# Performance work log

Hardware: AMD Instinct MI355X
Metric: run time of the kernel (lower is better)

## Reference

```python
import jax, jax.numpy as jnp
import numpy as np

ENC_DIM, PRED_DIM, JOINT_DIM, VOCAB = 512, 640, 512, 1024

def setup_inputs() -> dict:
    key = jax.random.key(0)
    ks = jax.random.split(key, 8)
    s = lambda d: 1.0 / np.sqrt(d)
    return {
        "enc_out": jax.random.normal(ks[0], (8, 256, ENC_DIM), jnp.float32),
        "pred_out": jax.random.normal(ks[1], (8, 64, PRED_DIM), jnp.float32),
        "W_enc": jax.random.uniform(ks[2], (ENC_DIM, JOINT_DIM), jnp.float32, -s(ENC_DIM), s(ENC_DIM)),
        "b_enc": jax.random.uniform(ks[3], (JOINT_DIM,), jnp.float32, -s(ENC_DIM), s(ENC_DIM)),
        "W_pred": jax.random.uniform(ks[4], (PRED_DIM, JOINT_DIM), jnp.float32, -s(PRED_DIM), s(PRED_DIM)),
        "b_pred": jax.random.uniform(ks[5], (JOINT_DIM,), jnp.float32, -s(PRED_DIM), s(PRED_DIM)),
        "W_joint": jax.random.uniform(ks[6], (JOINT_DIM, VOCAB), jnp.float32, -s(JOINT_DIM), s(JOINT_DIM)),
        "b_joint": jax.random.uniform(ks[7], (VOCAB,), jnp.float32, -s(JOINT_DIM), s(JOINT_DIM)),
    }

def reference(enc_out, pred_out, W_enc, b_enc, W_pred, b_pred, W_joint, b_joint):
    # (B,T,J) and (B,U,J) projections
    enc_p = jnp.einsum('btd,dj->btj', enc_out, W_enc) + b_enc
    pred_p = jnp.einsum('bud,dj->buj', pred_out, W_pred) + b_pred
    # broadcast add -> (B,T,U,J), tanh, project to vocab
    joint = jnp.tanh(enc_p[:, :, None, :] + pred_p[:, None, :, :])
    logits = jnp.einsum('btuj,jv->btuv', joint, W_joint) + b_joint
    return logits
```

## Files before the change

### kernel.cpp

```cpp
#include <hip/hip_runtime.h>
#include <hip/hip_bf16.h>
#include <stdint.h>

#define B_    8
#define T_    256
#define U_    64
#define JD    512
#define VD    1024
#define ROWS  (B_*T_*U_)
#define MTOT  (B_*T_)
#define UROWS (B_*U_)

typedef __attribute__((ext_vector_type(8))) short short8;
typedef __attribute__((ext_vector_type(4))) float f32x4;

__device__ __forceinline__ unsigned short f2bf(float f) {
  unsigned u = __float_as_uint(f);
  u += 0x7fffu + ((u >> 16) & 1u);
  return (unsigned short)(u >> 16);
}
__device__ __forceinline__ float fast_tanh(float x) {
  float e = __builtin_amdgcn_exp2f(x * 2.8853900817779268f);
  return 1.0f - 2.0f * __builtin_amdgcn_rcpf(e + 1.0f);
}

__global__ void __launch_bounds__(256) k_pack_w(
    const float* __restrict__ W, unsigned short* __restrict__ dst,
    int K, int N) {
  int t = blockIdx.x * blockDim.x + threadIdx.x;
  int total = (K * N) >> 3;
  if (t >= total) return;
  int lane = t & 63;
  int rest = t >> 6;
  int kch  = K >> 5;
  int kc   = rest % kch;
  int nt   = rest / kch;
  int krow = (kc << 5) + ((lane >> 4) << 3);
  int col  = (nt << 4) + (lane & 15);
  unsigned short v[8];
#pragma unroll
  for (int j = 0; j < 8; ++j) v[j] = f2bf(W[(size_t)(krow + j) * N + col]);
  uint4 o;
  o.x = v[0] | ((unsigned)v[1] << 16);
  o.y = v[2] | ((unsigned)v[3] << 16);
  o.z = v[4] | ((unsigned)v[5] << 16);
  o.w = v[6] | ((unsigned)v[7] << 16);
  *(uint4*)(dst + ((size_t)t << 3)) = o;
}

__global__ void __launch_bounds__(256) k_proj(
    const float* __restrict__ A, const unsigned short* __restrict__ Bp,
    const float* __restrict__ bias, float* __restrict__ C,
    int M, int K, int N) {
  int w    = (blockIdx.x * blockDim.x + threadIdx.x) >> 6;
  int lane = threadIdx.x & 63;
  int nw   = N >> 6;
  int wm   = w / nw, wn = w % nw;
  int m0   = wm << 4, n0 = wn << 6;
  if (m0 >= M) return;
  int kch = K >> 5;
  int q = lane >> 4, c = lane & 15;
  f32x4 acc[4] = {f32x4{0,0,0,0}, f32x4{0,0,0,0}, f32x4{0,0,0,0}, f32x4{0,0,0,0}};
  const float* arow = A + (size_t)(m0 + c) * K + (q << 3);
  for (int kc = 0; kc < kch; ++kc) {
    float4 a0 = *(const float4*)(arow + (kc << 5));
    float4 a1 = *(const float4*)(arow + (kc << 5) + 4);
    short8 a;
    a[0] = (short)f2bf(a0.x); a[1] = (short)f2bf(a0.y);
    a[2] = (short)f2bf(a0.z); a[3] = (short)f2bf(a0.w);
    a[4] = (short)f2bf(a1.x); a[5] = (short)f2bf(a1.y);
    a[6] = (short)f2bf(a1.z); a[7] = (short)f2bf(a1.w);
#pragma unroll
    for (int j = 0; j < 4; ++j) {
      size_t nt16 = (size_t)((n0 >> 4) + j);
      short8 b = *(const short8*)(Bp + (((nt16 * kch + kc) << 6) + lane) * 8);
      acc[j] = __builtin_amdgcn_mfma_f32_16x16x32_bf16(a, b, acc[j], 0, 0, 0);
    }
  }
#pragma unroll
  for (int j = 0; j < 4; ++j) {
    int col = n0 + (j << 4) + c;
    float bv = bias[col];
#pragma unroll
    for (int r = 0; r < 4; ++r) {
      int row = m0 + (q << 2) + r;
      C[(size_t)row * N + col] = acc[j][r] + bv;
    }
  }
}

__global__ void __launch_bounds__(256) k_tanh_pack(
    const float* __restrict__ enc_p, const float* __restrict__ pred_p,
    unsigned short* __restrict__ Ap) {
  int t    = blockIdx.x * blockDim.x + threadIdx.x;
  int lane = t & 63;
  int F    = t >> 6;
  int rb   = F >> 4, kc = F & 15;
  int r    = (rb << 4) + (lane & 15);
  int k0   = (kc << 5) + ((lane >> 4) << 3);
  const float* ep = enc_p  + ((size_t)(r >> 6) << 9) + k0;
  const float* pp = pred_p + ((size_t)(((r >> 14) << 6) + (r & 63)) << 9) + k0;
  float4 e0 = *(const float4*)ep, e1 = *(const float4*)(ep + 4);
  float4 p0 = *(const float4*)pp, p1 = *(const float4*)(pp + 4);
  unsigned short v[8];
  v[0] = f2bf(fast_tanh(e0.x + p0.x));
  v[1] = f2bf(fast_tanh(e0.y + p0.y));
  v[2] = f2bf(fast_tanh(e0.z + p0.z));
  v[3] = f2bf(fast_tanh(e0.w + p0.w));
  v[4] = f2bf(fast_tanh(e1.x + p1.x));
  v[5] = f2bf(fast_tanh(e1.y + p1.y));
  v[6] = f2bf(fast_tanh(e1.z + p1.z));
  v[7] = f2bf(fast_tanh(e1.w + p1.w));
  uint4 o;
  o.x = v[0] | ((unsigned)v[1] << 16);
  o.y = v[2] | ((unsigned)v[3] << 16);
  o.z = v[4] | ((unsigned)v[5] << 16);
  o.w = v[6] | ((unsigned)v[7] << 16);
  *(uint4*)(Ap + ((size_t)t << 3)) = o;
}

__global__ void __launch_bounds__(256) k_gemm3(
    const unsigned short* __restrict__ Ap, const unsigned short* __restrict__ Bp,
    const float* __restrict__ bias, float* __restrict__ out) {
  int bid  = blockIdx.x;
  int nt   = bid & 7;
  int mt   = bid >> 3;
  int w    = threadIdx.x >> 6, lane = threadIdx.x & 63;
  int wm   = w >> 1, wn = w & 1;
  int rb0  = (mt << 3) + (wm << 2);
  int nt0  = (nt << 3) + (wn << 2);
  const short8* a8 = (const short8*)Ap;
  const short8* b8 = (const short8*)Bp;

  f32x4 acc[4][4];
#pragma unroll
  for (int i = 0; i < 4; ++i)
#pragma unroll
    for (int j = 0; j < 4; ++j) acc[i][j] = f32x4{0, 0, 0, 0};

  short8 a[4], b[4], an[4], bn[4];
#pragma unroll
  for (int i = 0; i < 4; ++i) {
    a[i] = a8[(((size_t)(rb0 + i) * 16 + 0) << 6) + lane];
    b[i] = b8[(((size_t)(nt0 + i) * 16 + 0) << 6) + lane];
  }
#pragma unroll
  for (int kc = 0; kc < 16; ++kc) {
    if (kc < 15) {
#pragma unroll
      for (int i = 0; i < 4; ++i) {
        an[i] = a8[(((size_t)(rb0 + i) * 16 + kc + 1) << 6) + lane];
        bn[i] = b8[(((size_t)(nt0 + i) * 16 + kc + 1) << 6) + lane];
      }
    }
#pragma unroll
    for (int i = 0; i < 4; ++i)
#pragma unroll
      for (int j = 0; j < 4; ++j)
        acc[i][j] = __builtin_amdgcn_mfma_f32_16x16x32_bf16(a[i], b[j], acc[i][j], 0, 0, 0);
#pragma unroll
    for (int i = 0; i < 4; ++i) { a[i] = an[i]; b[i] = bn[i]; }
  }

  int q = lane >> 4, c = lane & 15;
#pragma unroll
  for (int j = 0; j < 4; ++j) {
    int col = ((nt0 + j) << 4) + c;
    float bv = bias[col];
#pragma unroll
    for (int i = 0; i < 4; ++i) {
      int row = ((rb0 + i) << 4) + (q << 2);
      size_t o = ((size_t)row << 10) + col;
#pragma unroll
      for (int r = 0; r < 4; ++r)
        out[o + ((size_t)r << 10)] = acc[i][j][r] + bv;
    }
  }
}

__global__ void __launch_bounds__(256) k_proj_naive(
    const float* __restrict__ A, const float* __restrict__ W,
    const float* __restrict__ bias, float* __restrict__ C,
    int M, int K, int N) {
  int t = blockIdx.x * blockDim.x + threadIdx.x;
  if (t >= M * N) return;
  int row = t / N, col = t % N;
  float s = bias[col];
  for (int k = 0; k < K; ++k)
    s += A[(size_t)row * K + k] * W[(size_t)k * N + col];
  C[t] = s;
}
__global__ void __launch_bounds__(256) k_joint_naive(
    const float* __restrict__ enc_p, const float* __restrict__ pred_p,
    const float* __restrict__ Wj, const float* __restrict__ bj,
    float* __restrict__ out) {
  __shared__ float jrow[JD];
  int gr = blockIdx.x;
  int bt = gr >> 6;
  int bu = ((gr >> 14) << 6) + (gr & 63);
  for (int k = threadIdx.x; k < JD; k += 256)
    jrow[k] = fast_tanh(enc_p[(size_t)bt * JD + k] + pred_p[(size_t)bu * JD + k]);
  __syncthreads();
  int v0 = threadIdx.x * 4;
  float s0 = bj[v0], s1 = bj[v0 + 1], s2 = bj[v0 + 2], s3 = bj[v0 + 3];
  for (int k = 0; k < JD; ++k) {
    float jv = jrow[k];
    const float* wr = Wj + (size_t)k * VD + v0;
    s0 += jv * wr[0];
    s1 += jv * wr[1];
    s2 += jv * wr[2];
    s3 += jv * wr[3];
  }
  size_t o = ((size_t)gr << 10) + v0;
  out[o] = s0; out[o + 1] = s1; out[o + 2] = s2; out[o + 3] = s3;
}

extern "C" void kernel_launch(void* const* d_in, const int* in_sizes, int n_in,
                              void* d_out, int out_size, void* d_ws, size_t ws_size,
                              hipStream_t stream) {
  const float* enc_out  = (const float*)d_in[0];
  const float* pred_out = (const float*)d_in[1];
  const float* W_enc    = (const float*)d_in[2];
  const float* b_enc    = (const float*)d_in[3];
  const float* W_pred   = (const float*)d_in[4];
  const float* b_pred   = (const float*)d_in[5];
  const float* W_joint  = (const float*)d_in[6];
  const float* b_joint  = (const float*)d_in[7];
  float* out = (float*)d_out;

  char* ws = (char*)d_ws;
  size_t off = 0;
  auto alloc = [&](size_t bytes) -> char* {
    char* p = ws + off;
    off += (bytes + 255) & ~(size_t)255;
    return p;
  };
  float* enc_p  = (float*)alloc((size_t)MTOT * JD * 4);
  float* pred_p = (float*)alloc((size_t)UROWS * JD * 4);
  size_t small_need = off;
  unsigned short* Wenc_p  = (unsigned short*)alloc((size_t)512 * 512 * 2);
  unsigned short* Wpred_p = (unsigned short*)alloc((size_t)640 * 512 * 2);
  unsigned short* Wjnt_p  = (unsigned short*)alloc((size_t)512 * 1024 * 2);
  unsigned short* Ap      = (unsigned short*)alloc((size_t)ROWS * JD * 2);
  size_t big_need = off;

  if (ws_size >= big_need) {
    k_pack_w<<<(512 * 512 / 8) / 256, 256, 0, stream>>>(W_enc, Wenc_p, 512, 512);
    k_pack_w<<<(640 * 512 / 8) / 256, 256, 0, stream>>>(W_pred, Wpred_p, 640, 512);
    k_pack_w<<<(512 * 1024 / 8) / 256, 256, 0, stream>>>(W_joint, Wjnt_p, 512, 1024);
    k_proj<<<(MTOT / 16) * (JD / 64) / 4, 256, 0, stream>>>(enc_out, Wenc_p, b_enc, enc_p, MTOT, 512, JD);
    k_proj<<<(UROWS / 16) * (JD / 64) / 4, 256, 0, stream>>>(pred_out, Wpred_p, b_pred, pred_p, UROWS, 640, JD);
    k_tanh_pack<<<((size_t)ROWS * JD / 8) / 256, 256, 0, stream>>>(enc_p, pred_p, Ap);
    k_gemm3<<<(ROWS / 128) * (VD / 128), 256, 0, stream>>>(Ap, Wjnt_p, b_joint, out);
  } else if (ws_size >= small_need) {
    k_proj_naive<<<(MTOT * JD + 255) / 256, 256, 0, stream>>>(enc_out, W_enc, b_enc, enc_p, MTOT, 512, JD);
    k_proj_naive<<<(UROWS * JD + 255) / 256, 256, 0, stream>>>(pred_out, W_pred, b_pred, pred_p, UROWS, 640, JD);
    k_joint_naive<<<ROWS, 256, 0, stream>>>(enc_p, pred_p, W_joint, b_joint, out);
  }
  (void)in_sizes; (void)n_in; (void)out_size;
}
```

Baseline: 959.4 us.

## Fuse tanh-pack into joint GEMM via LDS staging and merge small launches

The broadcast-add plus tanh plus bf16 pack is now computed per block into shared memory, chunk by chunk, inside the joint GEMM. This removes the large materialized Ap buffer and its global write and re-read. The three weight-pack launches and the two projection launches are each merged into a single kernel to cut launch overhead. The fused kernel uses 512-thread blocks with 128x256 tiles and syncthreads between the staging and MFMA phases. Tanh work is recomputed for each of the 4 N-tiles, and there is no double buffering, so staging may serialize with compute.

```diff
diff --git a/kernel.cpp b/kernel.cpp
--- a/kernel.cpp
+++ b/kernel.cpp
@@ -24,12 +24,9 @@
   return 1.0f - 2.0f * __builtin_amdgcn_rcpf(e + 1.0f);
 }
 
-__global__ void __launch_bounds__(256) k_pack_w(
-    const float* __restrict__ W, unsigned short* __restrict__ dst,
-    int K, int N) {
-  int t = blockIdx.x * blockDim.x + threadIdx.x;
-  int total = (K * N) >> 3;
-  if (t >= total) return;
+__device__ __forceinline__ void pack_w_body(const float* __restrict__ W,
+                                            unsigned short* __restrict__ dst,
+                                            int K, int N, int t) {
   int lane = t & 63;
   int rest = t >> 6;
   int kch  = K >> 5;
@@ -48,15 +45,24 @@
   *(uint4*)(dst + ((size_t)t << 3)) = o;
 }
 
-__global__ void __launch_bounds__(256) k_proj(
-    const float* __restrict__ A, const unsigned short* __restrict__ Bp,
-    const float* __restrict__ bias, float* __restrict__ C,
-    int M, int K, int N) {
-  int w    = (blockIdx.x * blockDim.x + threadIdx.x) >> 6;
-  int lane = threadIdx.x & 63;
-  int nw   = N >> 6;
-  int wm   = w / nw, wn = w % nw;
-  int m0   = wm << 4, n0 = wn << 6;
+__global__ void __launch_bounds__(256) k_pack_all(
+    const float* __restrict__ We, const float* __restrict__ Wp,
+    const float* __restrict__ Wj,
+    unsigned short* __restrict__ de, unsigned short* __restrict__ dp,
+    unsigned short* __restrict__ dj) {
+  int blk = blockIdx.x;
+  int tid = threadIdx.x;
+  if (blk < 128)      pack_w_body(We, de, 512, 512,  blk * 256 + tid);
+  else if (blk < 288) pack_w_body(Wp, dp, 640, 512,  (blk - 128) * 256 + tid);
+  else                pack_w_body(Wj, dj, 512, 1024, (blk - 288) * 256 + tid);
+}
+
+__device__ __forceinline__ void proj_body(const float* __restrict__ A,
+    const unsigned short* __restrict__ Bp, const float* __restrict__ bias,
+    float* __restrict__ C, int M, int K, int N, int w, int lane) {
+  int nw = N >> 6;
+  int wm = w / nw, wn = w % nw;
+  int m0 = wm << 4, n0 = wn << 6;
   if (m0 >= M) return;
   int kch = K >> 5;
   int q = lane >> 4, c = lane & 15;
@@ -89,48 +95,38 @@
   }
 }
 
-__global__ void __launch_bounds__(256) k_tanh_pack(
+__global__ void __launch_bounds__(256) k_proj_both(
+    const float* __restrict__ enc_out, const float* __restrict__ pred_out,
+    const unsigned short* __restrict__ Wep, const unsigned short* __restrict__ Wpp,
+    const float* __restrict__ b_enc, const float* __restrict__ b_pred,
+    float* __restrict__ enc_p, float* __restrict__ pred_p) {
+  int blk  = blockIdx.x;
+  int lane = threadIdx.x & 63;
+  int wloc = threadIdx.x >> 6;
+  if (blk < 256)
+    proj_body(enc_out,  Wep, b_enc,  enc_p,  MTOT,  512, JD, blk * 4 + wloc, lane);
+  else
+    proj_body(pred_out, Wpp, b_pred, pred_p, UROWS, 640, JD, (blk - 256) * 4 + wloc, lane);
+}
+
+__global__ void __launch_bounds__(512, 4) k_fused(
     const float* __restrict__ enc_p, const float* __restrict__ pred_p,
-    unsigned short* __restrict__ Ap) {
-  int t    = blockIdx.x * blockDim.x + threadIdx.x;
-  int lane = t & 63;
-  int F    = t >> 6;
-  int rb   = F >> 4, kc = F & 15;
-  int r    = (rb << 4) + (lane & 15);
-  int k0   = (kc << 5) + ((lane >> 4) << 3);
-  const float* ep = enc_p  + ((size_t)(r >> 6) << 9) + k0;
-  const float* pp = pred_p + ((size_t)(((r >> 14) << 6) + (r & 63)) << 9) + k0;
-  float4 e0 = *(const float4*)ep, e1 = *(const float4*)(ep + 4);
-  float4 p0 = *(const float4*)pp, p1 = *(const float4*)(pp + 4);
-  unsigned short v[8];
-  v[0] = f2bf(fast_tanh(e0.x + p0.x));
-  v[1] = f2bf(fast_tanh(e0.y + p0.y));
-  v[2] = f2bf(fast_tanh(e0.z + p0.z));
-  v[3] = f2bf(fast_tanh(e0.w + p0.w));
-  v[4] = f2bf(fast_tanh(e1.x + p1.x));
-  v[5] = f2bf(fast_tanh(e1.y + p1.y));
-  v[6] = f2bf(fast_tanh(e1.z + p1.z));
-  v[7] = f2bf(fast_tanh(e1.w + p1.w));
-  uint4 o;
-  o.x = v[0] | ((unsigned)v[1] << 16);
-  o.y = v[2] | ((unsigned)v[3] << 16);
-  o.z = v[4] | ((unsigned)v[5] << 16);
-  o.w = v[6] | ((unsigned)v[7] << 16);
-  *(uint4*)(Ap + ((size_t)t << 3)) = o;
-}
-
-__global__ void __launch_bounds__(256) k_gemm3(
-    const unsigned short* __restrict__ Ap, const unsigned short* __restrict__ Bp,
-    const float* __restrict__ bias, float* __restrict__ out) {
+    const unsigned short* __restrict__ Bp, const float* __restrict__ bias,
+    float* __restrict__ out) {
+  __shared__ unsigned short Alds[32 * 64 * 8];
+  const short8* a8 = (const short8*)Alds;
+  const short8* b8 = (const short8*)Bp;
+
   int bid  = blockIdx.x;
-  int nt   = bid & 7;
-  int mt   = bid >> 3;
-  int w    = threadIdx.x >> 6, lane = threadIdx.x & 63;
-  int wm   = w >> 1, wn = w & 1;
-  int rb0  = (mt << 3) + (wm << 2);
-  int nt0  = (nt << 3) + (wn << 2);
-  const short8* a8 = (const short8*)Ap;
-  const short8* b8 = (const short8*)Bp;
+  int nt   = bid & 3;
+  int mt   = bid >> 2;
+  int tid  = threadIdx.x;
+  int lane = tid & 63;
+  int w    = tid >> 6;
+  int wm   = w >> 2, wn = w & 3;
+  int rb0w = wm << 2;
+  int nt0w = (nt << 4) + (wn << 2);
+  int c15  = lane & 15, q8 = (lane >> 4) << 3;
 
   f32x4 acc[4][4];
 #pragma unroll
@@ -138,42 +134,66 @@
 #pragma unroll
     for (int j = 0; j < 4; ++j) acc[i][j] = f32x4{0, 0, 0, 0};
 
-  short8 a[4], b[4], an[4], bn[4];
-#pragma unroll
-  for (int i = 0; i < 4; ++i) {
-    a[i] = a8[(((size_t)(rb0 + i) * 16 + 0) << 6) + lane];
-    b[i] = b8[(((size_t)(nt0 + i) * 16 + 0) << 6) + lane];
-  }
-#pragma unroll
-  for (int kc = 0; kc < 16; ++kc) {
-    if (kc < 15) {
-#pragma unroll
-      for (int i = 0; i < 4; ++i) {
-        an[i] = a8[(((size_t)(rb0 + i) * 16 + kc + 1) << 6) + lane];
-        bn[i] = b8[(((size_t)(nt0 + i) * 16 + kc + 1) << 6) + lane];
-      }
-    }
-#pragma unroll
-    for (int i = 0; i < 4; ++i)
+  for (int ch = 0; ch < 4; ++ch) {
+    int kbase = ch << 7;
+#pragma unroll 2
+    for (int ff = 0; ff < 4; ++ff) {
+      int f   = w + (ff << 3);
+      int rb  = f >> 2, kcl = f & 3;
+      int r   = (mt << 7) + (rb << 4) + c15;
+      int k0  = kbase + (kcl << 5) + q8;
+      const float* ep = enc_p  + ((size_t)(r >> 6) << 9) + k0;
+      const float* pp = pred_p + ((size_t)(((r >> 14) << 6) + (r & 63)) << 9) + k0;
+      float4 e0 = *(const float4*)ep, e1 = *(const float4*)(ep + 4);
+      float4 p0 = *(const float4*)pp, p1 = *(const float4*)(pp + 4);
+      unsigned short v[8];
+      v[0] = f2bf(fast_tanh(e0.x + p0.x));
+      v[1] = f2bf(fast_tanh(e0.y + p0.y));
+      v[2] = f2bf(fast_tanh(e0.z + p0.z));
+      v[3] = f2bf(fast_tanh(e0.w + p0.w));
+      v[4] = f2bf(fast_tanh(e1.x + p1.x));
+      v[5] = f2bf(fast_tanh(e1.y + p1.y));
+      v[6] = f2bf(fast_tanh(e1.z + p1.z));
+      v[7] = f2bf(fast_tanh(e1.w + p1.w));
+      uint4 o;
+      o.x = v[0] | ((unsigned)v[1] << 16);
+      o.y = v[2] | ((unsigned)v[3] << 16);
+      o.z = v[4] | ((unsigned)v[5] << 16);
+      o.w = v[6] | ((unsigned)v[7] << 16);
+      *(uint4*)(Alds + ((((rb << 2) + kcl) << 6) + lane) * 8) = o;
+    }
+    __syncthreads();
+#pragma unroll
+    for (int kcl = 0; kcl < 4; ++kcl) {
+      int kc = (ch << 2) + kcl;
+      short8 a[4], b[4];
+#pragma unroll
+      for (int i = 0; i < 4; ++i)
+        a[i] = a8[(((rb0w + i) << 2) + kcl) * 64 + lane];
 #pragma unroll
       for (int j = 0; j < 4; ++j)
-        acc[i][j] = __builtin_amdgcn_mfma_f32_16x16x32_bf16(a[i], b[j], acc[i][j], 0, 0, 0);
-#pragma unroll
-    for (int i = 0; i < 4; ++i) { a[i] = an[i]; b[i] = bn[i]; }
-  }
-
-  int q = lane >> 4, c = lane & 15;
+        b[j] = b8[(((size_t)(nt0w + j) << 4) + kc) * 64 + lane];
+#pragma unroll
+      for (int i = 0; i < 4; ++i)
+#pragma unroll
+        for (int j = 0; j < 4; ++j)
+          acc[i][j] = __builtin_amdgcn_mfma_f32_16x16x32_bf16(a[i], b[j], acc[i][j], 0, 0, 0);
+    }
+    __syncthreads();
+  }
+
+  int q = lane >> 4;
 #pragma unroll
   for (int j = 0; j < 4; ++j) {
-    int col = ((nt0 + j) << 4) + c;
+    int col = ((nt0w + j) << 4) + c15;
     float bv = bias[col];
 #pragma unroll
     for (int i = 0; i < 4; ++i) {
-      int row = ((rb0 + i) << 4) + (q << 2);
+      int row = (mt << 7) + ((rb0w + i) << 4) + (q << 2);
       size_t o = ((size_t)row << 10) + col;
 #pragma unroll
-      for (int r = 0; r < 4; ++r)
-        out[o + ((size_t)r << 10)] = acc[i][j][r] + bv;
+      for (int rr = 0; rr < 4; ++rr)
+        out[o + ((size_t)rr << 10)] = acc[i][j][rr] + bv;
     }
   }
 }
@@ -241,17 +261,15 @@
   unsigned short* Wenc_p  = (unsigned short*)alloc((size_t)512 * 512 * 2);
   unsigned short* Wpred_p = (unsigned short*)alloc((size_t)640 * 512 * 2);
   unsigned short* Wjnt_p  = (unsigned short*)alloc((size_t)512 * 1024 * 2);
-  unsigned short* Ap      = (unsigned short*)alloc((size_t)ROWS * JD * 2);
   size_t big_need = off;
 
   if (ws_size >= big_need) {
-    k_pack_w<<<(512 * 512 / 8) / 256, 256, 0, stream>>>(W_enc, Wenc_p, 512, 512);
-    k_pack_w<<<(640 * 512 / 8) / 256, 256, 0, stream>>>(W_pred, Wpred_p, 640, 512);
-    k_pack_w<<<(512 * 1024 / 8) / 256, 256, 0, stream>>>(W_joint, Wjnt_p, 512, 1024);
-    k_proj<<<(MTOT / 16) * (JD / 64) / 4, 256, 0, stream>>>(enc_out, Wenc_p, b_enc, enc_p, MTOT, 512, JD);
-    k_proj<<<(UROWS / 16) * (JD / 64) / 4, 256, 0, stream>>>(pred_out, Wpred_p, b_pred, pred_p, UROWS, 640, JD);
-    k_tanh_pack<<<((size_t)ROWS * JD / 8) / 256, 256, 0, stream>>>(enc_p, pred_p, Ap);
-    k_gemm3<<<(ROWS / 128) * (VD / 128), 256, 0, stream>>>(Ap, Wjnt_p, b_joint, out);
+    k_pack_all<<<544, 256, 0, stream>>>(W_enc, W_pred, W_joint,
+                                        Wenc_p, Wpred_p, Wjnt_p);
+    k_proj_both<<<320, 256, 0, stream>>>(enc_out, pred_out, Wenc_p, Wpred_p,
+                                         b_enc, b_pred, enc_p, pred_p);
+    k_fused<<<(ROWS / 128) * (VD / 256), 512, 0, stream>>>(enc_p, pred_p,
+                                                           Wjnt_p, b_joint, out);
   } else if (ws_size >= small_need) {
     k_proj_naive<<<(MTOT * JD + 255) / 256, 256, 0, stream>>>(enc_out, W_enc, b_enc, enc_p, MTOT, 512, JD);
     k_proj_naive<<<(UROWS * JD + 255) / 256, 256, 0, stream>>>(pred_out, W_pred, b_pred, pred_p, UROWS, 640, JD);
```

Result: faster. 853.2 us (-11.1%).
